# Kernel tuning notes

Hardware: AMD Instinct MI355X
Metric: run time of the kernel (lower is better)

The kernel has to match this reference:

```python
import jax, jax.numpy as jnp
import numpy as np

ALPHA, BETA, GAMMA = 67.0, 3.0, 1.0  # DenseCRFParams3d defaults
NUM_ITERATIONS = 5


def _gauss_kernel(feats):
    # feats: (F, N) scaled features; returns (N, N) kernel exp(-0.5*||f_i-f_j||^2)
    sq = jnp.sum(feats * feats, axis=0)
    d2 = sq[:, None] + sq[None, :] - 2.0 * (feats.T @ feats)
    return jnp.exp(-0.5 * jnp.maximum(d2, 0.0))


def _filter(K, q_ln):
    # K: (N, N) symmetric Gaussian kernel; q_ln: (L, N)
    # normalized Gaussian filtering (splat/blur/slice with slice normalization)
    out = q_ln @ K  # (L, N); K symmetric
    norm = jnp.sum(K, axis=0)  # K @ ones
    return out / norm[None, :]


def setup_inputs() -> dict:
    key = jax.random.key(0)
    k1, k2 = jax.random.split(key)
    L, C, D, W, H = 21, 3, 16, 16, 16
    image = jax.random.uniform(k1, (1, C, D, W, H), dtype=jnp.float32)
    logits = jax.random.normal(k2, (1, L, D, W, H), dtype=jnp.float32)
    spatial_ker_weights = 3.0 * jnp.eye(L, dtype=jnp.float32)
    bilateral_ker_weights = 5.0 * jnp.eye(L, dtype=jnp.float32)
    compatibility_matrix = jnp.eye(L, dtype=jnp.float32)
    return {
        "image": image,
        "logits": logits,
        "spatial_ker_weights": spatial_ker_weights,
        "bilateral_ker_weights": bilateral_ker_weights,
        "compatibility_matrix": compatibility_matrix,
    }


def reference(image, logits, spatial_ker_weights, bilateral_ker_weights, compatibility_matrix):
    img = image[0]            # (C, D, W, H)
    unary = logits[0]         # (L, D, W, H)
    C, D, W, H = img.shape
    L = unary.shape[0]
    N = D * W * H

    # voxel coordinates (3, N)
    zz, yy, xx = jnp.meshgrid(jnp.arange(D), jnp.arange(W), jnp.arange(H), indexing="ij")
    pos = jnp.stack([zz, yy, xx]).reshape(3, N).astype(jnp.float32)

    # kernels are fixed across iterations -> build once
    K_sp = _gauss_kernel(pos / GAMMA)                                   # spatial kernel
    feats_bi = jnp.concatenate([pos / ALPHA, img.reshape(C, N) / BETA], axis=0)
    K_bi = _gauss_kernel(feats_bi)                                      # bilateral kernel

    cur = unary
    for _ in range(NUM_ITERATIONS):
        q = jax.nn.softmax(cur, axis=0).reshape(L, N)
        spatial_out = spatial_ker_weights @ _filter(K_sp, q)
        bilateral_out = bilateral_ker_weights @ _filter(K_bi, q)
        msg = compatibility_matrix @ (spatial_out + bilateral_out)
        cur = msg.reshape(L, D, W, H) + unary
    return cur[None]  # (1, L, D, W, H)
```

## Files before the change

kernel.cpp:

```cpp
#include <hip/hip_runtime.h>

#define L 21
#define NVOX 4096
#define ITERS 5
#define NU 210
#define UPAD 224
#define VPB 16
#define NSPLIT 16
#define USPL 14

__global__ __launch_bounds__(256) void phase_ab(
    const float* __restrict__ img, const float* __restrict__ logits,
    const float* __restrict__ Wsp, const float* __restrict__ Wbi,
    const float* __restrict__ Wc,
    float* __restrict__ Phi, float* __restrict__ nsp, float* __restrict__ q,
    float* __restrict__ cu, float* __restrict__ W1, float* __restrict__ W2,
    float* __restrict__ A2p)
{
    const int tid = threadIdx.x;
    const int bid = blockIdx.x;
    if (bid < 64) {
        int lane = tid & 63, w = tid >> 6;
        int i = bid * 64 + lane;
        int z = i >> 8, yy = (i >> 4) & 15, xx = i & 15;
        const float ia = 1.0f / 67.0f, ib = 1.0f / 3.0f;
        float f[6];
        f[0] = (float)z * ia; f[1] = (float)yy * ia; f[2] = (float)xx * ia;
        f[3] = img[i] * ib; f[4] = img[NVOX + i] * ib; f[5] = img[2 * NVOX + i] * ib;
        float p[6][5];
#pragma unroll
        for (int c = 0; c < 6; c++) {
            p[c][0] = 1.f;
#pragma unroll
            for (int k = 1; k < 5; k++) p[c][k] = p[c][k - 1] * f[c];
        }
        float hsv = 0.5f * (f[0]*f[0] + f[1]*f[1] + f[2]*f[2] +
                            f[3]*f[3] + f[4]*f[4] + f[5]*f[5]);
        float e0 = __expf(-hsv);
        int ulo = w * 56, uhi = ulo + 56;
        int u = 0;
        for (int a0 = 0; a0 <= 4; a0++)
        for (int a1 = 0; a1 <= 4 - a0; a1++)
        for (int a2 = 0; a2 <= 4 - a0 - a1; a2++)
        for (int a3 = 0; a3 <= 4 - a0 - a1 - a2; a3++)
        for (int a4 = 0; a4 <= 4 - a0 - a1 - a2 - a3; a4++)
        for (int a5 = 0; a5 <= 4 - a0 - a1 - a2 - a3 - a4; a5++) {
            if (u >= ulo && u < uhi)
                Phi[(size_t)u * NVOX + i] =
                    e0 * p[0][a0] * p[1][a1] * p[2][a2] * p[3][a3] * p[4][a4] * p[5][a5];
            u++;
        }
        if (w == 3)
            for (int uz = NU; uz < UPAD; uz++) Phi[(size_t)uz * NVOX + i] = 0.f;
        if (w == 0) {
            float hz = 0.f, hy = 0.f, hx = 0.f;
            for (int t = 0; t < 16; t++) {
                float dz = (float)(z - t), dy = (float)(yy - t), dx = (float)(xx - t);
                hz += __expf(-0.5f * dz * dz);
                hy += __expf(-0.5f * dy * dy);
                hx += __expf(-0.5f * dx * dx);
            }
            nsp[i] = hz * hy * hx;
        }
        if (w == 1) {
            float vals[L]; float mx = -1e30f;
#pragma unroll
            for (int l = 0; l < L; l++) { vals[l] = logits[l * NVOX + i]; mx = fmaxf(mx, vals[l]); }
            float sum = 0.f;
#pragma unroll
            for (int l = 0; l < L; l++) { vals[l] = __expf(vals[l] - mx); sum += vals[l]; }
            float inv = 1.f / sum;
#pragma unroll
            for (int l = 0; l < L; l++) q[l * NVOX + i] = vals[l] * inv;
        }
    } else if (bid == 64) {
        for (int e = tid; e < L * L; e += 256) {
            int r = e / L, c = e % L;
            float s1 = 0.f, s2 = 0.f;
            for (int k = 0; k < L; k++) {
                float wc = Wc[r * L + k];
                s1 = fmaf(wc, Wsp[k * L + c], s1);
                s2 = fmaf(wc, Wbi[k * L + c], s2);
            }
            W1[e] = s1; W2[e] = s2;
        }
    } else if (bid == 65) {
        const float invf[5] = {1.f, 1.f, 0.5f, 1.f / 6.f, 1.f / 24.f};
        float mine = 0.f;
        int v = 0;
        for (int a0 = 0; a0 <= 4; a0++)
        for (int a1 = 0; a1 <= 4 - a0; a1++)
        for (int a2 = 0; a2 <= 4 - a0 - a1; a2++)
        for (int a3 = 0; a3 <= 4 - a0 - a1 - a2; a3++)
        for (int a4 = 0; a4 <= 4 - a0 - a1 - a2 - a3; a4++)
        for (int a5 = 0; a5 <= 4 - a0 - a1 - a2 - a3 - a4; a5++) {
            if (v == tid)
                mine = invf[a0] * invf[a1] * invf[a2] * invf[a3] * invf[a4] * invf[a5];
            v++;
        }
        cu[tid] = mine;
    } else {
        for (int e = tid; e < 4 * L * (UPAD - NU); e += 256) {
            int w = e / (L * (UPAD - NU));
            int r = e % (L * (UPAD - NU));
            int m = r / (UPAD - NU);
            int u = NU + r % (UPAD - NU);
            A2p[(size_t)(w * L + m) * UPAD + u] = 0.f;
        }
    }
}

__global__ __launch_bounds__(256) void phase_p2(
    const float* __restrict__ Phi, const float* __restrict__ q,
    const float* __restrict__ cu, const float* __restrict__ W2,
    float* __restrict__ A2p, float* __restrict__ spv,
    float* __restrict__ bnorm, int it0)
{
    __shared__ float buf[NVOX];
    __shared__ float tmp[NVOX];
    __shared__ float g[16];
    const int tid = threadIdx.x;
    const int bid = blockIdx.x;
    if (bid < NU) {
        int lane = tid & 63, w = tid >> 6;
        const float* ph = Phi + (size_t)bid * NVOX + w * 1024;
        const float* qq = q + w * 1024;
        float acc[L];
#pragma unroll
        for (int m = 0; m < L; m++) acc[m] = 0.f;
#pragma unroll 2
        for (int ii = lane; ii < 1024; ii += 64) {
            float p = ph[ii];
#pragma unroll
            for (int m = 0; m < L; m++)
                acc[m] = fmaf(qq[m * NVOX + ii], p, acc[m]);
        }
#pragma unroll
        for (int off = 32; off >= 1; off >>= 1)
#pragma unroll
            for (int m = 0; m < L; m++)
                acc[m] += __shfl_xor(acc[m], off);
        if (lane < L) {
            float dot = 0.f;
#pragma unroll
            for (int m = 0; m < L; m++)
                dot = fmaf(W2[lane * L + m], acc[m], dot);
            A2p[(size_t)(w * L + lane) * UPAD + bid] = cu[bid] * dot;
        }
    } else if (bid < NU + L) {
        int l = bid - NU;
        if (tid < 16) g[tid] = __expf(-0.5f * (float)(tid * tid));
        for (int k = 0; k < 16; k++)
            buf[tid + 256 * k] = q[l * NVOX + tid + 256 * k];
        __syncthreads();
        for (int k = 0; k < 16; k++) {
            int idx = tid + 256 * k;
            int x = idx & 15, base = idx & ~15;
            float ssum = 0.f;
#pragma unroll
            for (int t = 0; t < 16; t++) {
                int d = x - t; d = d < 0 ? -d : d;
                ssum += g[d] * buf[base + t];
            }
            tmp[idx] = ssum;
        }
        __syncthreads();
        for (int k = 0; k < 16; k++) {
            int idx = tid + 256 * k;
            int y = (idx >> 4) & 15, base = idx & ~(15 << 4);
            float ssum = 0.f;
#pragma unroll
            for (int t = 0; t < 16; t++) {
                int d = y - t; d = d < 0 ? -d : d;
                ssum += g[d] * tmp[base + (t << 4)];
            }
            buf[idx] = ssum;
        }
        __syncthreads();
        for (int k = 0; k < 16; k++) {
            int idx = tid + 256 * k;
            int z = idx >> 8, base = idx & 255;
            float ssum = 0.f;
#pragma unroll
            for (int t = 0; t < 16; t++) {
                int d = z - t; d = d < 0 ? -d : d;
                ssum += g[d] * buf[base + (t << 8)];
            }
            spv[l * NVOX + idx] = ssum;
        }
    } else if (it0) {
        int wg = (bid - (NU + L)) * 4 + (tid >> 6);
        int lane = tid & 63;
        for (int u = wg; u < UPAD; u += 25 * 4) {
            const float* row = Phi + (size_t)u * NVOX;
            float ssum = 0.f;
            for (int ii = lane; ii < NVOX; ii += 64) ssum += row[ii];
#pragma unroll
            for (int off = 32; off >= 1; off >>= 1) ssum += __shfl_xor(ssum, off);
            if (lane == 0) bnorm[u] = cu[u] * ssum;
        }
    }
}

__global__ __launch_bounds__(256) void phase_p3(
    const float* __restrict__ Phi, const float* __restrict__ A2p,
    const float* __restrict__ bnorm, const float* __restrict__ spv,
    const float* __restrict__ nsp, const float* __restrict__ W1,
    const float* __restrict__ logits, float* __restrict__ q,
    float* __restrict__ out, int last)
{
    __shared__ float sA[L * UPAD];
    __shared__ float sN[UPAD];
    __shared__ float red[22][NSPLIT][VPB];
    __shared__ float sw1[L * L];
    __shared__ float sspn[VPB][22];
    __shared__ float scur[VPB][22];
    const int tid = threadIdx.x;
    const int bid = blockIdx.x;
    const int v = tid & (VPB - 1);
    const int s = tid >> 4;
    const int i16 = bid * VPB + v;

    for (int e = tid; e < L * UPAD; e += 256)
        sA[e] = A2p[e] + A2p[L * UPAD + e] +
                A2p[2 * L * UPAD + e] + A2p[3 * L * UPAD + e];
    for (int e = tid; e < UPAD; e += 256) sN[e] = bnorm[e];
    for (int e = tid; e < L * L; e += 256) sw1[e] = W1[e];
    {
        float rsp = 1.f / nsp[i16];
        for (int m = s; m < L; m += NSPLIT)
            sspn[v][m] = spv[m * NVOX + i16] * rsp;
    }
    __syncthreads();
    float acc[L], accN = 0.f;
#pragma unroll
    for (int m = 0; m < L; m++) acc[m] = 0.f;
    int u0 = s * USPL;
    for (int uu = 0; uu < USPL; uu++) {
        float p = Phi[(size_t)(u0 + uu) * NVOX + i16];
#pragma unroll
        for (int m = 0; m < L; m++)
            acc[m] = fmaf(sA[m * UPAD + u0 + uu], p, acc[m]);
        accN = fmaf(sN[u0 + uu], p, accN);
    }
#pragma unroll
    for (int m = 0; m < L; m++) red[m][s][v] = acc[m];
    red[21][s][v] = accN;
    __syncthreads();
    float b21 = 0.f;
#pragma unroll
    for (int ss = 0; ss < NSPLIT; ss++) b21 += red[21][ss][v];
    float rbi = 1.f / b21;
    for (int l = s; l < L; l += NSPLIT) {
        float bl = 0.f;
#pragma unroll
        for (int ss = 0; ss < NSPLIT; ss++) bl += red[l][ss][v];
        float r = bl * rbi;
#pragma unroll
        for (int m = 0; m < L; m++)
            r = fmaf(sw1[l * L + m], sspn[v][m], r);
        r += logits[l * NVOX + i16];
        scur[v][l] = r;
        if (last) out[l * NVOX + i16] = r;
    }
    __syncthreads();
    if (!last && tid < VPB) {
        int i = bid * VPB + tid;
        float vals[L]; float mx = -1e30f;
#pragma unroll
        for (int l = 0; l < L; l++) { vals[l] = scur[tid][l]; mx = fmaxf(mx, vals[l]); }
        float sum = 0.f;
#pragma unroll
        for (int l = 0; l < L; l++) { vals[l] = __expf(vals[l] - mx); sum += vals[l]; }
        float inv = 1.f / sum;
#pragma unroll
        for (int l = 0; l < L; l++) q[l * NVOX + i] = vals[l] * inv;
    }
}

extern "C" void kernel_launch(void* const* d_in, const int* in_sizes, int n_in,
                              void* d_out, int out_size, void* d_ws, size_t ws_size,
                              hipStream_t stream) {
    const float* image  = (const float*)d_in[0];
    const float* logits = (const float*)d_in[1];
    const float* Wsp    = (const float*)d_in[2];
    const float* Wbi    = (const float*)d_in[3];
    const float* Wc     = (const float*)d_in[4];
    float* out = (float*)d_out;

    char* ws = (char*)d_ws;
    float* Phi   = (float*)ws; ws += (size_t)UPAD * NVOX * sizeof(float);
    float* nsp   = (float*)ws; ws += (size_t)NVOX * sizeof(float);
    float* q     = (float*)ws; ws += (size_t)L * NVOX * sizeof(float);
    float* spv   = (float*)ws; ws += (size_t)L * NVOX * sizeof(float);
    float* A2p   = (float*)ws; ws += (size_t)4 * L * UPAD * sizeof(float);
    float* bnorm = (float*)ws; ws += (size_t)UPAD * sizeof(float);
    float* cu    = (float*)ws; ws += (size_t)256 * sizeof(float);
    float* W1    = (float*)ws; ws += (size_t)L * L * sizeof(float);
    float* W2    = (float*)ws; ws += (size_t)L * L * sizeof(float);

    phase_ab<<<67, 256, 0, stream>>>(image, logits, Wsp, Wbi, Wc,
                                     Phi, nsp, q, cu, W1, W2, A2p);
    for (int it = 0; it < ITERS; it++) {
        int nb2 = (it == 0) ? 256 : (NU + L);
        phase_p2<<<nb2, 256, 0, stream>>>(Phi, q, cu, W2, A2p, spv, bnorm,
                                          it == 0 ? 1 : 0);
        phase_p3<<<256, 256, 0, stream>>>(Phi, A2p, bnorm, spv, nsp, W1,
                                          logits, q, out,
                                          it == ITERS - 1 ? 1 : 0);
    }
}
```

Measured before the change: 195.5 us.

## Split Phi-q projection across two blocks per basis with float4 loads and atomics

The bilateral projection stage now runs two blocks per polynomial basis function instead of one, each covering half the voxels. It reads Phi and q with float4 vector loads and accumulates partial results into a single A2 buffer with atomicAdd, replacing the four-way partial buffer that phase_p3 had to sum. A double-buffered A2 is zeroed for the next iteration inside phase_p3. The intent is more parallelism and memory-level throughput in phase_p2, at the cost of atomic contention and non-deterministic summation order.

```diff
diff --git a/kernel.cpp b/kernel.cpp
--- a/kernel.cpp
+++ b/kernel.cpp
@@ -8,6 +8,7 @@
 #define VPB 16
 #define NSPLIT 16
 #define USPL 14
+#define NG1 420
 
 __global__ __launch_bounds__(256) void phase_ab(
     const float* __restrict__ img, const float* __restrict__ logits,
@@ -15,7 +16,7 @@
     const float* __restrict__ Wc,
     float* __restrict__ Phi, float* __restrict__ nsp, float* __restrict__ q,
     float* __restrict__ cu, float* __restrict__ W1, float* __restrict__ W2,
-    float* __restrict__ A2p)
+    float* __restrict__ A2)
 {
     const int tid = threadIdx.x;
     const int bid = blockIdx.x;
@@ -100,20 +101,14 @@
         }
         cu[tid] = mine;
     } else {
-        for (int e = tid; e < 4 * L * (UPAD - NU); e += 256) {
-            int w = e / (L * (UPAD - NU));
-            int r = e % (L * (UPAD - NU));
-            int m = r / (UPAD - NU);
-            int u = NU + r % (UPAD - NU);
-            A2p[(size_t)(w * L + m) * UPAD + u] = 0.f;
-        }
+        for (int e = tid; e < 2 * L * UPAD; e += 256) A2[e] = 0.f;
     }
 }
 
 __global__ __launch_bounds__(256) void phase_p2(
     const float* __restrict__ Phi, const float* __restrict__ q,
     const float* __restrict__ cu, const float* __restrict__ W2,
-    float* __restrict__ A2p, float* __restrict__ spv,
+    float* __restrict__ A2cur, float* __restrict__ spv,
     float* __restrict__ bnorm, int it0)
 {
     __shared__ float buf[NVOX];
@@ -121,19 +116,25 @@
     __shared__ float g[16];
     const int tid = threadIdx.x;
     const int bid = blockIdx.x;
-    if (bid < NU) {
+    if (bid < NG1) {
+        int u = bid >> 1;
         int lane = tid & 63, w = tid >> 6;
-        const float* ph = Phi + (size_t)bid * NVOX + w * 1024;
-        const float* qq = q + w * 1024;
+        int i0 = (bid & 1) * 2048 + w * 512;
+        const float4* ph = (const float4*)(Phi + (size_t)u * NVOX + i0);
         float acc[L];
 #pragma unroll
         for (int m = 0; m < L; m++) acc[m] = 0.f;
-#pragma unroll 2
-        for (int ii = lane; ii < 1024; ii += 64) {
-            float p = ph[ii];
-#pragma unroll
-            for (int m = 0; m < L; m++)
-                acc[m] = fmaf(qq[m * NVOX + ii], p, acc[m]);
+#pragma unroll
+        for (int rep = 0; rep < 2; rep++) {
+            int ii = lane + rep * 64;
+            float4 p = ph[ii];
+#pragma unroll
+            for (int m = 0; m < L; m++) {
+                float4 qv = ((const float4*)(q + m * NVOX + i0))[ii];
+                float d = fmaf(qv.x, p.x, fmaf(qv.y, p.y,
+                          fmaf(qv.z, p.z, qv.w * p.w)));
+                acc[m] += d;
+            }
         }
 #pragma unroll
         for (int off = 32; off >= 1; off >>= 1)
@@ -145,10 +146,10 @@
 #pragma unroll
             for (int m = 0; m < L; m++)
                 dot = fmaf(W2[lane * L + m], acc[m], dot);
-            A2p[(size_t)(w * L + lane) * UPAD + bid] = cu[bid] * dot;
-        }
-    } else if (bid < NU + L) {
-        int l = bid - NU;
+            atomicAdd(&A2cur[lane * UPAD + u], cu[u] * dot);
+        }
+    } else if (bid < NG1 + L) {
+        int l = bid - NG1;
         if (tid < 16) g[tid] = __expf(-0.5f * (float)(tid * tid));
         for (int k = 0; k < 16; k++)
             buf[tid + 256 * k] = q[l * NVOX + tid + 256 * k];
@@ -189,7 +190,7 @@
             spv[l * NVOX + idx] = ssum;
         }
     } else if (it0) {
-        int wg = (bid - (NU + L)) * 4 + (tid >> 6);
+        int wg = (bid - (NG1 + L)) * 4 + (tid >> 6);
         int lane = tid & 63;
         for (int u = wg; u < UPAD; u += 25 * 4) {
             const float* row = Phi + (size_t)u * NVOX;
@@ -203,11 +204,11 @@
 }
 
 __global__ __launch_bounds__(256) void phase_p3(
-    const float* __restrict__ Phi, const float* __restrict__ A2p,
-    const float* __restrict__ bnorm, const float* __restrict__ spv,
-    const float* __restrict__ nsp, const float* __restrict__ W1,
-    const float* __restrict__ logits, float* __restrict__ q,
-    float* __restrict__ out, int last)
+    const float* __restrict__ Phi, const float* __restrict__ A2cur,
+    float* __restrict__ A2next, const float* __restrict__ bnorm,
+    const float* __restrict__ spv, const float* __restrict__ nsp,
+    const float* __restrict__ W1, const float* __restrict__ logits,
+    float* __restrict__ q, float* __restrict__ out, int last)
 {
     __shared__ float sA[L * UPAD];
     __shared__ float sN[UPAD];
@@ -221,9 +222,11 @@
     const int s = tid >> 4;
     const int i16 = bid * VPB + v;
 
-    for (int e = tid; e < L * UPAD; e += 256)
-        sA[e] = A2p[e] + A2p[L * UPAD + e] +
-                A2p[2 * L * UPAD + e] + A2p[3 * L * UPAD + e];
+    {
+        int e = bid * 256 + tid;
+        if (e < L * UPAD) A2next[e] = 0.f;
+    }
+    for (int e = tid; e < L * UPAD; e += 256) sA[e] = A2cur[e];
     for (int e = tid; e < UPAD; e += 256) sN[e] = bnorm[e];
     for (int e = tid; e < L * L; e += 256) sw1[e] = W1[e];
     {
@@ -293,20 +296,22 @@
     float* nsp   = (float*)ws; ws += (size_t)NVOX * sizeof(float);
     float* q     = (float*)ws; ws += (size_t)L * NVOX * sizeof(float);
     float* spv   = (float*)ws; ws += (size_t)L * NVOX * sizeof(float);
-    float* A2p   = (float*)ws; ws += (size_t)4 * L * UPAD * sizeof(float);
+    float* A2    = (float*)ws; ws += (size_t)2 * L * UPAD * sizeof(float);
     float* bnorm = (float*)ws; ws += (size_t)UPAD * sizeof(float);
     float* cu    = (float*)ws; ws += (size_t)256 * sizeof(float);
     float* W1    = (float*)ws; ws += (size_t)L * L * sizeof(float);
     float* W2    = (float*)ws; ws += (size_t)L * L * sizeof(float);
 
     phase_ab<<<67, 256, 0, stream>>>(image, logits, Wsp, Wbi, Wc,
-                                     Phi, nsp, q, cu, W1, W2, A2p);
+                                     Phi, nsp, q, cu, W1, W2, A2);
     for (int it = 0; it < ITERS; it++) {
-        int nb2 = (it == 0) ? 256 : (NU + L);
-        phase_p2<<<nb2, 256, 0, stream>>>(Phi, q, cu, W2, A2p, spv, bnorm,
+        float* A2cur  = A2 + (it & 1) * L * UPAD;
+        float* A2next = A2 + ((it + 1) & 1) * L * UPAD;
+        int nb2 = (it == 0) ? 466 : (NG1 + L);
+        phase_p2<<<nb2, 256, 0, stream>>>(Phi, q, cu, W2, A2cur, spv, bnorm,
                                           it == 0 ? 1 : 0);
-        phase_p3<<<256, 256, 0, stream>>>(Phi, A2p, bnorm, spv, nsp, W1,
-                                          logits, q, out,
+        phase_p3<<<256, 256, 0, stream>>>(Phi, A2cur, A2next, bnorm, spv, nsp,
+                                          W1, logits, q, out,
                                           it == ITERS - 1 ? 1 : 0);
     }
 }
```

Result: no change. 197.1 us (+0.8%).
